# Performance work log

Hardware: AMD Instinct MI355X
Metric: run time of the kernel (lower is better)

Reference implementation:

```python
import jax, jax.numpy as jnp
import numpy as np

N = 70000
H = 8
E = 1120000
B = 8


def setup_inputs() -> dict:
    key = jax.random.key(0)
    ks = jax.random.split(key, 12)
    inp = {
        'calcium_t': jax.random.normal(ks[0], (B, N), jnp.float32),
        'hidden': jax.random.normal(ks[1], (B, N, H), jnp.float32),
        'src': jax.random.randint(ks[2], (E,), 0, N, jnp.int32),
        'tgt': jax.random.randint(ks[3], (E,), 0, N, jnp.int32),
        'W_z_values': jax.random.normal(ks[4], (E, H), jnp.float32) * 0.01,
        'W_r_values': jax.random.normal(ks[5], (E, H), jnp.float32) * 0.01,
        'W_h_values': jax.random.normal(ks[6], (E, H), jnp.float32) * 0.01,
        'U_z': jax.random.normal(ks[7], (N, H, H), jnp.float32) * 0.01,
        'U_r': jax.random.normal(ks[8], (N, H, H), jnp.float32) * 0.01,
        'U_h': jax.random.normal(ks[9], (N, H, H), jnp.float32) * 0.01,
        'b_z': jnp.zeros((N, H), jnp.float32),
        'b_r': jnp.zeros((N, H), jnp.float32),
        'b_h': jnp.zeros((N, H), jnp.float32),
        'output_projection': jax.random.normal(ks[10], (H,), jnp.float32),
    }
    return inp


def _sparse_matmul(values, src, tgt, calcium):
    # out[b, n, h] = sum over edges e with tgt[e]==n of values[e,h]*calcium[b,src[e]]
    # (identical to coalesced COO mm: duplicate (row,col) values are summed)
    gathered = calcium.T[src]                      # (E, B)
    contrib = gathered[:, :, None] * values[:, None, :]  # (E, B, H)
    out = jax.ops.segment_sum(contrib, tgt, num_segments=N)  # (N, B, H)
    return jnp.transpose(out, (1, 0, 2))           # (B, N, H)


def reference(calcium_t, hidden, src, tgt, W_z_values, W_r_values, W_h_values,
              U_z, U_r, U_h, b_z, b_r, b_h, output_projection):
    inp_z = _sparse_matmul(W_z_values, src, tgt, calcium_t)
    inp_r = _sparse_matmul(W_r_values, src, tgt, calcium_t)
    inp_h = _sparse_matmul(W_h_values, src, tgt, calcium_t)

    rec_z = jnp.einsum('bnh,nhi->bni', hidden, U_z)
    rec_r = jnp.einsum('bnh,nhi->bni', hidden, U_r)
    z = jax.nn.sigmoid(inp_z + rec_z + b_z[None])
    r = jax.nn.sigmoid(inp_r + rec_r + b_r[None])

    rec_h = jnp.einsum('bnh,nhi->bni', r * hidden, U_h)
    h_tilde = jnp.tanh(inp_h + rec_h + b_h[None])

    hidden_new = (1.0 - z) * hidden + z * h_tilde
    calcium_t1 = jax.nn.relu(jnp.einsum('bnh,h->bn', hidden_new, output_projection))
    return calcium_t1, hidden_new
```

## Files before the change

### kernel.cpp

```cpp
#include <hip/hip_runtime.h>


__device__ __forceinline__ float fast_sigmoid(float x) {
    return 1.0f / (1.0f + __expf(-x));
}
__device__ __forceinline__ float fast_tanh(float x) {
    return 2.0f / (1.0f + __expf(-2.0f * x)) - 1.0f;
}

#define FMA8F(acc, v0, v1, c)                                                  \
    {                                                                          \
        acc[0] += (v0).x * (c); acc[1] += (v0).y * (c);                        \
        acc[2] += (v0).z * (c); acc[3] += (v0).w * (c);                        \
        acc[4] += (v1).x * (c); acc[5] += (v1).y * (c);                        \
        acc[6] += (v1).z * (c); acc[7] += (v1).w * (c);                        \
    }

__global__ void hist_kernel(const int* __restrict__ tgt, int* __restrict__ cnt,
                            int* __restrict__ rank, int E) {
    int i = blockIdx.x * blockDim.x + threadIdx.x;
    int base = i * 4;
    if (base + 3 < E) {
        int4 t = *(const int4*)(tgt + base);
        int4 r;
        r.x = atomicAdd(&cnt[t.x], 1);
        r.y = atomicAdd(&cnt[t.y], 1);
        r.z = atomicAdd(&cnt[t.z], 1);
        r.w = atomicAdd(&cnt[t.w], 1);
        *(int4*)(rank + base) = r;
    } else {
        for (int k = base; k < E; ++k) rank[k] = atomicAdd(&cnt[tgt[k]], 1);
    }
}

__global__ __launch_bounds__(256) void alloc_kernel(const int* __restrict__ cnt,
                                                    int2* __restrict__ rowCnt,
                                                    int* __restrict__ cursor,
                                                    const float* __restrict__ cal,
                                                    float* __restrict__ calT, int N) {
    __shared__ int waveSum[4];
    const int n = blockIdx.x * 256 + threadIdx.x;
    const int lane = threadIdx.x & 63;
    const int wid = threadIdx.x >> 6;
    int c = (n < N) ? cnt[n] : 0;
    int pre = c;
#pragma unroll
    for (int off = 1; off < 64; off <<= 1) {
        int v = __shfl_up(pre, off, 64);
        if (lane >= off) pre += v;
    }
    if (lane == 63) waveSum[wid] = pre;
    __syncthreads();
    if (threadIdx.x == 0) {
        int s0 = waveSum[0], s1 = waveSum[1], s2 = waveSum[2], s3 = waveSum[3];
        int base = atomicAdd(cursor, s0 + s1 + s2 + s3);
        waveSum[0] = base;
        waveSum[1] = base + s0;
        waveSum[2] = base + s0 + s1;
        waveSum[3] = base + s0 + s1 + s2;
    }
    __syncthreads();
    if (n < N) {
        rowCnt[n] = make_int2(waveSum[wid] + (pre - c), c);
        float v[8];
#pragma unroll
        for (int b = 0; b < 8; ++b) v[b] = cal[(size_t)b * N + n];
        float4* o = (float4*)(calT + (size_t)n * 8);
        o[0] = make_float4(v[0], v[1], v[2], v[3]);
        o[1] = make_float4(v[4], v[5], v[6], v[7]);
    }
}

__global__ __launch_bounds__(256) void edge_prep(
    const int* __restrict__ src, const int* __restrict__ tgt,
    const int* __restrict__ rank, const int2* __restrict__ rowCnt,
    const float* __restrict__ calT, int* __restrict__ eIdxCSR,
    float* __restrict__ calE, int E) {
    int i = blockIdx.x * 256 + threadIdx.x;
    if (i >= E) return;
    int t = tgt[i];
    eIdxCSR[rowCnt[t].x + rank[i]] = i;
    const float4* ca = (const float4*)(calT + (size_t)src[i] * 8);
    float4 c0 = ca[0], c1 = ca[1];
    float4* o = (float4*)(calE + (size_t)i * 8);
    o[0] = c0;
    o[1] = c1;
}

__device__ __forceinline__ float rscatter(float v[8], int lane) {
    const bool s0 = (lane & 8) != 0;
    const bool s1 = (lane & 16) != 0;
    const bool s2 = (lane & 32) != 0;
    float w0, w1, w2, w3, x0, x1;
    { float k = s0 ? v[1] : v[0], g = s0 ? v[0] : v[1]; w0 = k + __shfl_xor(g, 8, 64); }
    { float k = s0 ? v[3] : v[2], g = s0 ? v[2] : v[3]; w1 = k + __shfl_xor(g, 8, 64); }
    { float k = s0 ? v[5] : v[4], g = s0 ? v[4] : v[5]; w2 = k + __shfl_xor(g, 8, 64); }
    { float k = s0 ? v[7] : v[6], g = s0 ? v[6] : v[7]; w3 = k + __shfl_xor(g, 8, 64); }
    { float k = s1 ? w1 : w0, g = s1 ? w0 : w1; x0 = k + __shfl_xor(g, 16, 64); }
    { float k = s1 ? w3 : w2, g = s1 ? w2 : w3; x1 = k + __shfl_xor(g, 16, 64); }
    float k = s2 ? x1 : x0, g = s2 ? x0 : x1;
    return k + __shfl_xor(g, 32, 64);
}

__global__ __launch_bounds__(256) void gru_main(
    const float* __restrict__ hidden,
    const int* __restrict__ eIdxCSR, const float* __restrict__ calE,
    const float* __restrict__ Wz, const float* __restrict__ Wr,
    const float* __restrict__ Wh,
    const float* __restrict__ Uz, const float* __restrict__ Ur,
    const float* __restrict__ Uh, const float* __restrict__ bz,
    const float* __restrict__ br, const float* __restrict__ bh,
    const float* __restrict__ proj, const int2* __restrict__ rowCnt,
    float* __restrict__ outCal, float* __restrict__ outHid, int N) {
    const int lane = threadIdx.x & 63;
    const int n = blockIdx.x * 4 + (threadIdx.x >> 6);
    if (n >= N) return;
    const int s = lane >> 3;
    const int b = lane & 7;

    const int2 rc = rowCnt[n];
    const int start = rc.x;
    const int end = rc.x + rc.y;

    const float hvS = hidden[((b * N + n) << 3) + s];
    const int ub = (n << 6) + (s << 3);
    float4 uz0 = *(const float4*)(Uz + ub);
    float4 uz1 = *(const float4*)(Uz + ub + 4);
    float4 ur0 = *(const float4*)(Ur + ub);
    float4 ur1 = *(const float4*)(Ur + ub + 4);
    float4 uh0 = *(const float4*)(Uh + ub);
    float4 uh1 = *(const float4*)(Uh + ub + 4);
    const float bzS = bz[(n << 3) + s];
    const float brS = br[(n << 3) + s];
    const float bhS = bh[(n << 3) + s];
    const float pjS = proj[s];

    float az[8] = {0, 0, 0, 0, 0, 0, 0, 0};
    float ar[8] = {0, 0, 0, 0, 0, 0, 0, 0};
    float ah[8] = {0, 0, 0, 0, 0, 0, 0, 0};

    for (int j = start + s; j < end; j += 8) {
        int e = eIdxCSR[j];
        size_t eo = (size_t)e << 3;
        const float4* wz4 = (const float4*)(Wz + eo);
        const float4* wr4 = (const float4*)(Wr + eo);
        const float4* wh4 = (const float4*)(Wh + eo);
        float4 z0 = wz4[0], z1 = wz4[1];
        float4 r0 = wr4[0], r1 = wr4[1];
        float4 h0 = wh4[0], h1 = wh4[1];
        float c = calE[eo + b];
        FMA8F(az, z0, z1, c);
        FMA8F(ar, r0, r1, c);
        FMA8F(ah, h0, h1, c);
    }

    az[0] += hvS * uz0.x; az[1] += hvS * uz0.y; az[2] += hvS * uz0.z; az[3] += hvS * uz0.w;
    az[4] += hvS * uz1.x; az[5] += hvS * uz1.y; az[6] += hvS * uz1.z; az[7] += hvS * uz1.w;
    ar[0] += hvS * ur0.x; ar[1] += hvS * ur0.y; ar[2] += hvS * ur0.z; ar[3] += hvS * ur0.w;
    ar[4] += hvS * ur1.x; ar[5] += hvS * ur1.y; ar[6] += hvS * ur1.z; ar[7] += hvS * ur1.w;

    float AZ = rscatter(az, lane);
    float AR = rscatter(ar, lane);
    float z = fast_sigmoid(AZ + bzS);
    float r = fast_sigmoid(AR + brS);
    float rhS = r * hvS;

    ah[0] += rhS * uh0.x; ah[1] += rhS * uh0.y; ah[2] += rhS * uh0.z; ah[3] += rhS * uh0.w;
    ah[4] += rhS * uh1.x; ah[5] += rhS * uh1.y; ah[6] += rhS * uh1.z; ah[7] += rhS * uh1.w;
    float AH = rscatter(ah, lane);
    float ht = fast_tanh(AH + bhS);
    float hn = (1.0f - z) * hvS + z * ht;

    float cv = hn * pjS;
    cv += __shfl_xor(cv, 8, 64);
    cv += __shfl_xor(cv, 16, 64);
    cv += __shfl_xor(cv, 32, 64);

    outHid[((b * N + n) << 3) + s] = hn;
    if (s == 0) outCal[b * N + n] = fmaxf(cv, 0.0f);
}

extern "C" void kernel_launch(void* const* d_in, const int* in_sizes, int n_in,
                              void* d_out, int out_size, void* d_ws, size_t ws_size,
                              hipStream_t stream) {
    const float* calcium = (const float*)d_in[0];
    const float* hidden  = (const float*)d_in[1];
    const int*   src     = (const int*)d_in[2];
    const int*   tgt     = (const int*)d_in[3];
    const float* Wz      = (const float*)d_in[4];
    const float* Wr      = (const float*)d_in[5];
    const float* Wh      = (const float*)d_in[6];
    const float* Uz      = (const float*)d_in[7];
    const float* Ur      = (const float*)d_in[8];
    const float* Uh      = (const float*)d_in[9];
    const float* bz      = (const float*)d_in[10];
    const float* br      = (const float*)d_in[11];
    const float* bh      = (const float*)d_in[12];
    const float* proj    = (const float*)d_in[13];

    const int E = in_sizes[2];
    const int H = in_sizes[13];
    const int N = in_sizes[10] / H;
    (void)n_in; (void)out_size; (void)ws_size;

    float* out = (float*)d_out;
    float* outCal = out;
    float* outHid = out + (size_t)in_sizes[0];

    char* ws = (char*)d_ws;
    int*   cnt     = (int*)ws;
    int*   cursor  = (int*)(ws + (448 << 10));
    int2*  rowCnt  = (int2*)(ws + (512 << 10));
    int*   rank    = (int*)(ws + (1280 << 10));
    float* calT    = (float*)(ws + (6 << 20));
    int*   eIdxCSR = (int*)(ws + (9 << 20));
    float* calE    = (float*)(ws + (14 << 20));

    hipMemsetAsync(ws, 0, (448 << 10) + 4, stream);

    hist_kernel<<<((E + 3) / 4 + 255) / 256, 256, 0, stream>>>(tgt, cnt, rank, E);
    alloc_kernel<<<(N + 255) / 256, 256, 0, stream>>>(
        cnt, rowCnt, cursor, calcium, calT, N);
    edge_prep<<<(E + 255) / 256, 256, 0, stream>>>(
        src, tgt, rank, rowCnt, calT, eIdxCSR, calE, E);
    gru_main<<<(N + 3) / 4, 256, 0, stream>>>(
        hidden, eIdxCSR, calE, Wz, Wr, Wh, Uz, Ur, Uh, bz, br, bh, proj,
        rowCnt, outCal, outHid, N);
}
```

Measured before the change: 208.9 us.

## Pack edge weights and calcium into bf16 records for the gather loop

The edge prep kernel now rounds each edge's W_z/W_r/W_h values and its gathered calcium row to bf16 and packs them into one contiguous 64-byte record. The main GRU kernel then reads a single record per edge instead of three separate fp32 weight rows plus a calcium row, and it prefetches the next CSR edge index one iteration ahead. This halves the bytes of the random-access gather in the main loop but adds a full pass over the weights in the prep kernel. Precision drops to bf16 for the input-side products, which may exceed tolerance.

```diff
diff --git a/kernel.cpp b/kernel.cpp
--- a/kernel.cpp
+++ b/kernel.cpp
@@ -8,12 +8,29 @@
     return 2.0f / (1.0f + __expf(-2.0f * x)) - 1.0f;
 }
 
-#define FMA8F(acc, v0, v1, c)                                                  \
+__device__ __forceinline__ unsigned bfr(float x) {
+    unsigned u = __float_as_uint(x);
+    return (u + 0x7fffu + ((u >> 16) & 1u)) >> 16;
+}
+__device__ __forceinline__ uint4 pack8(float4 a, float4 b) {
+    uint4 r;
+    r.x = bfr(a.x) | (bfr(a.y) << 16);
+    r.y = bfr(a.z) | (bfr(a.w) << 16);
+    r.z = bfr(b.x) | (bfr(b.y) << 16);
+    r.w = bfr(b.z) | (bfr(b.w) << 16);
+    return r;
+}
+
+#define BFMA(acc, p, c)                                                        \
     {                                                                          \
-        acc[0] += (v0).x * (c); acc[1] += (v0).y * (c);                        \
-        acc[2] += (v0).z * (c); acc[3] += (v0).w * (c);                        \
-        acc[4] += (v1).x * (c); acc[5] += (v1).y * (c);                        \
-        acc[6] += (v1).z * (c); acc[7] += (v1).w * (c);                        \
+        acc[0] += __uint_as_float((p).x << 16) * (c);                          \
+        acc[1] += __uint_as_float((p).x & 0xffff0000u) * (c);                  \
+        acc[2] += __uint_as_float((p).y << 16) * (c);                          \
+        acc[3] += __uint_as_float((p).y & 0xffff0000u) * (c);                  \
+        acc[4] += __uint_as_float((p).z << 16) * (c);                          \
+        acc[5] += __uint_as_float((p).z & 0xffff0000u) * (c);                  \
+        acc[6] += __uint_as_float((p).w << 16) * (c);                          \
+        acc[7] += __uint_as_float((p).w & 0xffff0000u) * (c);                  \
     }
 
 __global__ void hist_kernel(const int* __restrict__ tgt, int* __restrict__ cnt,
@@ -71,20 +88,25 @@
     }
 }
 
-__global__ __launch_bounds__(256) void edge_prep(
+__global__ __launch_bounds__(256) void edge_pack(
     const int* __restrict__ src, const int* __restrict__ tgt,
     const int* __restrict__ rank, const int2* __restrict__ rowCnt,
-    const float* __restrict__ calT, int* __restrict__ eIdxCSR,
-    float* __restrict__ calE, int E) {
+    const float* __restrict__ Wz, const float* __restrict__ Wr,
+    const float* __restrict__ Wh, const float* __restrict__ calT,
+    uint4* __restrict__ recs, int* __restrict__ eIdxCSR, int E) {
     int i = blockIdx.x * 256 + threadIdx.x;
     if (i >= E) return;
     int t = tgt[i];
     eIdxCSR[rowCnt[t].x + rank[i]] = i;
-    const float4* ca = (const float4*)(calT + (size_t)src[i] * 8);
-    float4 c0 = ca[0], c1 = ca[1];
-    float4* o = (float4*)(calE + (size_t)i * 8);
-    o[0] = c0;
-    o[1] = c1;
+    const float4* wz4 = (const float4*)(Wz + (size_t)i * 8);
+    const float4* wr4 = (const float4*)(Wr + (size_t)i * 8);
+    const float4* wh4 = (const float4*)(Wh + (size_t)i * 8);
+    const float4* ca4 = (const float4*)(calT + (size_t)src[i] * 8);
+    uint4* rp = recs + (size_t)i * 4;
+    rp[0] = pack8(wz4[0], wz4[1]);
+    rp[1] = pack8(wr4[0], wr4[1]);
+    rp[2] = pack8(wh4[0], wh4[1]);
+    rp[3] = pack8(ca4[0], ca4[1]);
 }
 
 __device__ __forceinline__ float rscatter(float v[8], int lane) {
@@ -103,10 +125,8 @@
 }
 
 __global__ __launch_bounds__(256) void gru_main(
-    const float* __restrict__ hidden,
-    const int* __restrict__ eIdxCSR, const float* __restrict__ calE,
-    const float* __restrict__ Wz, const float* __restrict__ Wr,
-    const float* __restrict__ Wh,
+    const float* __restrict__ hidden, const uint4* __restrict__ recs,
+    const int* __restrict__ eIdxCSR,
     const float* __restrict__ Uz, const float* __restrict__ Ur,
     const float* __restrict__ Uh, const float* __restrict__ bz,
     const float* __restrict__ br, const float* __restrict__ bh,
@@ -139,19 +159,23 @@
     float ar[8] = {0, 0, 0, 0, 0, 0, 0, 0};
     float ah[8] = {0, 0, 0, 0, 0, 0, 0, 0};
 
-    for (int j = start + s; j < end; j += 8) {
-        int e = eIdxCSR[j];
-        size_t eo = (size_t)e << 3;
-        const float4* wz4 = (const float4*)(Wz + eo);
-        const float4* wr4 = (const float4*)(Wr + eo);
-        const float4* wh4 = (const float4*)(Wh + eo);
-        float4 z0 = wz4[0], z1 = wz4[1];
-        float4 r0 = wr4[0], r1 = wr4[1];
-        float4 h0 = wh4[0], h1 = wh4[1];
-        float c = calE[eo + b];
-        FMA8F(az, z0, z1, c);
-        FMA8F(ar, r0, r1, c);
-        FMA8F(ah, h0, h1, c);
+    const unsigned short* recsH = (const unsigned short*)recs;
+    int j = start + s;
+    int e = (j < end) ? eIdxCSR[j] : 0;
+    while (j < end) {
+        int jn = j + 8;
+        int en = (jn < end) ? eIdxCSR[jn] : 0;
+        const uint4* rp = recs + (size_t)e * 4;
+        uint4 pz = rp[0];
+        uint4 pr = rp[1];
+        uint4 ph = rp[2];
+        unsigned cb = recsH[((size_t)e << 5) + 24 + b];
+        float c = __uint_as_float(cb << 16);
+        BFMA(az, pz, c);
+        BFMA(ar, pr, c);
+        BFMA(ah, ph, c);
+        j = jn;
+        e = en;
     }
 
     az[0] += hvS * uz0.x; az[1] += hvS * uz0.y; az[2] += hvS * uz0.z; az[3] += hvS * uz0.w;
@@ -214,16 +238,16 @@
     int*   rank    = (int*)(ws + (1280 << 10));
     float* calT    = (float*)(ws + (6 << 20));
     int*   eIdxCSR = (int*)(ws + (9 << 20));
-    float* calE    = (float*)(ws + (14 << 20));
+    uint4* recs    = (uint4*)(ws + (14 << 20));
 
     hipMemsetAsync(ws, 0, (448 << 10) + 4, stream);
 
     hist_kernel<<<((E + 3) / 4 + 255) / 256, 256, 0, stream>>>(tgt, cnt, rank, E);
     alloc_kernel<<<(N + 255) / 256, 256, 0, stream>>>(
         cnt, rowCnt, cursor, calcium, calT, N);
-    edge_prep<<<(E + 255) / 256, 256, 0, stream>>>(
-        src, tgt, rank, rowCnt, calT, eIdxCSR, calE, E);
+    edge_pack<<<(E + 255) / 256, 256, 0, stream>>>(
+        src, tgt, rank, rowCnt, Wz, Wr, Wh, calT, recs, eIdxCSR, E);
     gru_main<<<(N + 3) / 4, 256, 0, stream>>>(
-        hidden, eIdxCSR, calE, Wz, Wr, Wh, Uz, Ur, Uh, bz, br, bh, proj,
+        hidden, recs, eIdxCSR, Uz, Ur, Uh, bz, br, bh, proj,
         rowCnt, outCal, outHid, N);
 }
```

New measurement: 214.5 us. 1.03x slower.
